# Kernel tuning notes

Hardware: AMD Instinct MI355X
Metric: run time of the kernel (lower is better)

## Reference

```python
import jax, jax.numpy as jnp
import numpy as np

# sorted irreps after merging time embedding: 144x0e + 128x1o
S = 144   # scalar (0e) multiplicity: 16 (time embedding) + 128 (node feature scalars)
V = 128   # vector (1o) multiplicity
FS = 128  # scalar part of node features
INV_SQRT3 = 1.0 / np.sqrt(3.0)  # component-normalized CG for 1o x 1o -> 0e (dot/sqrt(3))


def setup_inputs() -> dict:
    key = jax.random.key(0)
    ks = jax.random.split(key, 9)
    N = 4096
    return {
        "flat_node_features": jax.random.normal(ks[0], (N, FS + 3 * V), jnp.float32),
        "flat_times": jax.random.uniform(ks[1], (N, 1), jnp.float32),
        # time embedding o3.Linear 1x0e -> 16x0e
        "W_t": jax.random.normal(ks[2], (1, 16), jnp.float32),
        # linear_1: per-l block linear on 144x0e + 128x1o
        "W1_s": jax.random.normal(ks[3], (S, S), jnp.float32),
        "W1_v": jax.random.normal(ks[4], (V, V), jnp.float32),
        # TensorSquare path weights: strict-upper triangle = 'u<v' paths, diagonal = 'uuw' paths
        "Wss": jax.random.normal(ks[5], (S, S, S), jnp.float32),  # 0e x 0e -> 0e
        "Wsv": jax.random.normal(ks[6], (S, V, V), jnp.float32),  # 0e x 1o -> 1o ('uvw')
        "Wvv": jax.random.normal(ks[7], (V, V, S), jnp.float32),  # 1o x 1o -> 0e
        # linear_2: 128x1o -> 1x1o
        "W2": jax.random.normal(ks[8], (V, 1), jnp.float32),
    }


def _forward(feat, times, W_t, W1_s, W1_v, Wss, Wsv, Wvv, W2):
    N = feat.shape[0]
    # time embedding (fan_in = 1) + concat + (identity) permutation into sorted irreps
    emb = times @ W_t                                   # [N,16]
    s = jnp.concatenate([emb, feat[:, :FS]], axis=1)    # [N,S] scalars (0e)
    v = feat[:, FS:].reshape(N, V, 3)                   # [N,V,3] vectors (1o)

    # linear_1 (irreps-wise, fan_in normalized)
    s1 = (s @ W1_s) / np.sqrt(S)                        # [N,S]
    v1 = jnp.einsum("num,uw->nwm", v, W1_v) / np.sqrt(V)  # [N,V,3]

    # ---- TensorSquare (sorted -> sorted) ----
    mask_s = jnp.triu(jnp.ones((S, S), s1.dtype), 1)
    mask_v = jnp.triu(jnp.ones((V, V), v1.dtype), 1)

    # path A: 0e x 0e -> 0e, 'u<v'
    WssU = Wss * mask_s[:, :, None]
    tA = jnp.einsum("nvw,nv->nw", jnp.einsum("nu,uvw->nvw", s1, WssU), s1)
    tA = tA / np.sqrt(S * (S - 1) / 2)
    # path B: 0e x 0e -> 0e, 'uuw' (diagonal u==v)
    tB = jnp.einsum("nu,uw->nw", s1 * s1, jnp.einsum("uuw->uw", Wss)) / np.sqrt(S)
    # path C: 1o x 1o -> 0e, 'u<v'  (CG = dot/sqrt(3))
    D = jnp.einsum("num,nvm->nuv", v1, v1) * INV_SQRT3   # [N,V,V]
    tC = jnp.einsum("nuv,uvw->nw", D, Wvv * mask_v[:, :, None]) / np.sqrt(V * (V - 1) / 2)
    # path D: 1o x 1o -> 0e, 'uuw'
    norms = jnp.sum(v1 * v1, axis=-1) * INV_SQRT3        # [N,V]
    tD = jnp.einsum("nu,uw->nw", norms, jnp.einsum("uuw->uw", Wvv)) / np.sqrt(V)
    s2 = (tA + tB + tC + tD) / np.sqrt(4.0)              # 4 paths into 0e

    # path E: 0e x 1o -> 1o, 'uvw' (single path; CG identity under component norm)
    tmp = jnp.einsum("nu,uvw->nvw", s1, Wsv) / np.sqrt(S * V)  # [N,V,V]
    v2 = jnp.einsum("nvw,nvm->nwm", tmp, v1)             # [N,V,3]

    # gated nonlinearity: silu on scalar (l=0) channel only
    s3 = jax.nn.silu(s2)
    del s3  # scalars do not feed linear_2 (irreps_out = 1x1o has no 0e path)

    # linear_2: 128x1o -> 1x1o
    out = jnp.einsum("num,uk->nkm", v2, W2)[:, 0, :] / np.sqrt(V)  # [N,3]
    return out


def reference(flat_node_features, flat_times, W_t, W1_s, W1_v, Wss, Wsv, Wvv, W2):
    return _forward(flat_node_features, flat_times, W_t, W1_s, W1_v, Wss, Wsv, Wvv, W2)
```

## Files before the change

### kernel.cpp

```cpp
#include <hip/hip_runtime.h>
#include <hip/hip_bf16.h>
#include <math.h>


#define S 144
#define V 128

typedef __attribute__((ext_vector_type(8))) short bf16x8;
typedef __attribute__((ext_vector_type(4))) float f32x4;

__global__ __launch_bounds__(256) void k1_D(const float* __restrict__ Wsv,
                                            const float* __restrict__ W2,
                                            float* __restrict__ D) {
    const int wave = threadIdx.x >> 6;
    const int lane = threadIdx.x & 63;
    const int uv = blockIdx.x * 4 + wave;
    const float2* src = (const float2*)Wsv + (size_t)uv * 64;
    const float2* w2 = (const float2*)W2;
    float2 a = src[lane];
    float2 w = w2[lane];
    float acc = a.x * w.x + a.y * w.y;
#pragma unroll
    for (int off = 1; off < 64; off <<= 1)
        acc += __shfl_xor(acc, off, 64);
    if (lane == 0) D[uv] = acc;
}

__global__ __launch_bounds__(256) void k23_Mb(const float* __restrict__ D,
                                              const float* __restrict__ W1s,
                                              const float* __restrict__ W1v,
                                              const float* __restrict__ Wt,
                                              unsigned short* __restrict__ Mt,
                                              float* __restrict__ b) {
    __shared__ float w1v[V * 129];
    __shared__ float wrow[S];
    __shared__ float Fpart[4][V];
    __shared__ float Fsh[V];
    const int tid = threadIdx.x;
    const int q = blockIdx.x;

    {
        const float4* W1v4 = (const float4*)W1v;
        for (int i = tid; i < V * V / 4; i += 256) {
            const float4 t = W1v4[i];
            const int base = i * 4;
            float* dst = &w1v[(base >> 7) * 129 + (base & 127)];
            dst[0] = t.x; dst[1] = t.y; dst[2] = t.z; dst[3] = t.w;
        }
    }
    if (tid < S) {
        if (q < V) {
            wrow[tid] = W1s[(16 + q) * S + tid];
        } else {
            float acc = 0.f;
#pragma unroll
            for (int p = 0; p < 16; ++p)
                acc = fmaf(Wt[p], W1s[p * S + tid], acc);
            wrow[tid] = acc;
        }
    }
    __syncthreads();

    {
        const int w = tid >> 6, t = tid & 63;
        float fx = 0.f, fy = 0.f;
#pragma unroll 6
        for (int u = 36 * w; u < 36 * w + 36; ++u) {
            const float wr = wrow[u];
            const float2 dv = *(const float2*)&D[u * V + 2 * t];
            fx = fmaf(wr, dv.x, fx);
            fy = fmaf(wr, dv.y, fy);
        }
        Fpart[w][2 * t + 0] = fx;
        Fpart[w][2 * t + 1] = fy;
    }
    __syncthreads();
    if (tid < V)
        Fsh[tid] = (Fpart[0][tid] + Fpart[1][tid]) + (Fpart[2][tid] + Fpart[3][tid]);
    __syncthreads();

    if (tid < V) {
        const float scale = 1.0f / (144.0f * 128.0f * sqrtf(128.0f));
        float m0 = 0.f, m1 = 0.f, m2 = 0.f, m3 = 0.f;
#pragma unroll 8
        for (int v = 0; v < V; v += 4) {
            m0 = fmaf(Fsh[v + 0], w1v[tid * 129 + v + 0], m0);
            m1 = fmaf(Fsh[v + 1], w1v[tid * 129 + v + 1], m1);
            m2 = fmaf(Fsh[v + 2], w1v[tid * 129 + v + 2], m2);
            m3 = fmaf(Fsh[v + 3], w1v[tid * 129 + v + 3], m3);
        }
        const float r = ((m0 + m1) + (m2 + m3)) * scale;
        if (q < V) {
            const __hip_bfloat16 h = __float2bfloat16(r);
            Mt[tid * V + q] = *(const unsigned short*)&h;
        } else {
            b[tid] = r;
        }
    }
}

__global__ __launch_bounds__(256) void k4_mfma(const float* __restrict__ feat,
                                               const float* __restrict__ times,
                                               const unsigned short* __restrict__ Mtg,
                                               const float* __restrict__ bg,
                                               float* __restrict__ out) {
    __shared__ unsigned short Msh[V][136];
    __shared__ unsigned short srow[16][136];
    __shared__ float tsh[16];
    __shared__ float red[4][16][3];
    const int tid = threadIdx.x;
    const int wave = tid >> 6;
    const int lane = tid & 63;
    const int n0 = blockIdx.x * 16;

    {
        const uint4* src = (const uint4*)Mtg;
#pragma unroll
        for (int i = 0; i < 8; ++i) {
            const int idx = tid + 256 * i;
            const int r = idx >> 4;
            const int c8 = (idx & 15) * 8;
            *(uint4*)&Msh[r][c8] = src[idx];
        }
    }
    {
        const int r = tid >> 4, q0 = (tid & 15) * 8;
        const float* p = feat + (size_t)(n0 + r) * 512 + q0;
        const float4 f0 = *(const float4*)(p);
        const float4 f1 = *(const float4*)(p + 4);
        __hip_bfloat162 p0 = __float22bfloat162_rn(make_float2(f0.x, f0.y));
        __hip_bfloat162 p1 = __float22bfloat162_rn(make_float2(f0.z, f0.w));
        __hip_bfloat162 p2 = __float22bfloat162_rn(make_float2(f1.x, f1.y));
        __hip_bfloat162 p3 = __float22bfloat162_rn(make_float2(f1.z, f1.w));
        uint4 pk;
        pk.x = *(const unsigned*)&p0;
        pk.y = *(const unsigned*)&p1;
        pk.z = *(const unsigned*)&p2;
        pk.w = *(const unsigned*)&p3;
        *(uint4*)&srow[r][q0] = pk;
    }
    if (tid < 16) tsh[tid] = times[n0 + tid];
    const int mrow = lane & 15;
    const int kch = lane >> 4;
    const float bc0 = bg[32 * wave + mrow];
    const float bc1 = bg[32 * wave + 16 + mrow];
    __syncthreads();

    f32x4 acc0 = {0.f, 0.f, 0.f, 0.f};
    f32x4 acc1 = {0.f, 0.f, 0.f, 0.f};
#pragma unroll
    for (int kk = 0; kk < 4; ++kk) {
        const bf16x8 af = *(const bf16x8*)&srow[mrow][kk * 32 + kch * 8];
        const bf16x8 bf0 = *(const bf16x8*)&Msh[32 * wave + mrow][kk * 32 + kch * 8];
        const bf16x8 bf1 = *(const bf16x8*)&Msh[32 * wave + 16 + mrow][kk * 32 + kch * 8];
        acc0 = __builtin_amdgcn_mfma_f32_16x16x32_bf16(af, bf0, acc0, 0, 0, 0);
        acc1 = __builtin_amdgcn_mfma_f32_16x16x32_bf16(af, bf1, acc1, 0, 0, 0);
    }

    float pm[4][3];
#pragma unroll
    for (int i = 0; i < 4; ++i) {
        const int nr = kch * 4 + i;
        const float t = tsh[nr];
        const float h0 = acc0[i] + t * bc0;
        const float h1 = acc1[i] + t * bc1;
        const float* vp0 = feat + (size_t)(n0 + nr) * 512 + V + 3 * (32 * wave + mrow);
        const float* vp1 = vp0 + 48;
#pragma unroll
        for (int m = 0; m < 3; ++m)
            pm[i][m] = vp0[m] * h0 + vp1[m] * h1;
    }
#pragma unroll
    for (int i = 0; i < 4; ++i) {
#pragma unroll
        for (int m = 0; m < 3; ++m) {
            float v = pm[i][m];
            v += __shfl_xor(v, 1, 64);
            v += __shfl_xor(v, 2, 64);
            v += __shfl_xor(v, 4, 64);
            v += __shfl_xor(v, 8, 64);
            pm[i][m] = v;
        }
        if (mrow == 0) {
            const int nr = kch * 4 + i;
            red[wave][nr][0] = pm[i][0];
            red[wave][nr][1] = pm[i][1];
            red[wave][nr][2] = pm[i][2];
        }
    }
    __syncthreads();
    if (tid < 48) {
        const int nr = tid / 3, m = tid % 3;
        out[(size_t)(n0 + nr) * 3 + m] =
            red[0][nr][m] + red[1][nr][m] + red[2][nr][m] + red[3][nr][m];
    }
}

extern "C" void kernel_launch(void* const* d_in, const int* in_sizes, int n_in,
                              void* d_out, int out_size, void* d_ws, size_t ws_size,
                              hipStream_t stream) {
    const float* feat  = (const float*)d_in[0];
    const float* times = (const float*)d_in[1];
    const float* Wt    = (const float*)d_in[2];
    const float* W1s   = (const float*)d_in[3];
    const float* W1v   = (const float*)d_in[4];
    const float* Wsv   = (const float*)d_in[6];
    const float* W2    = (const float*)d_in[8];

    float* ws = (float*)d_ws;
    float* D  = ws;
    unsigned short* Mt = (unsigned short*)(ws + 18432);
    float* b  = ws + 18432 + 8192;

    k1_D<<<dim3(4608), dim3(256), 0, stream>>>(Wsv, W2, D);
    k23_Mb<<<dim3(129), dim3(256), 0, stream>>>(D, W1s, W1v, Wt, Mt, b);
    k4_mfma<<<dim3(256), dim3(256), 0, stream>>>(feat, times, Mt, b, (float*)d_out);
}
```

Measured before the change: 18.71 us.

## Fuse weight-reduction and M-building kernels with atomic counter handoff

Merges the Wsv·W2 reduction kernel and the M/b construction kernel into one launch. 144 producer blocks each reduce one u-slice with float4 loads, then increment a global counter. 129 consumer blocks stage W1v and wrow while producers run, and spin on the counter before reading D. This removes a kernel launch boundary and overlaps consumer staging with producer work. In exchange it adds a memset launch and relies on all producer blocks being resident or scheduled ahead of consumers to avoid deadlock.

```diff
diff --git a/kernel.cpp b/kernel.cpp
--- a/kernel.cpp
+++ b/kernel.cpp
@@ -9,92 +9,114 @@
 typedef __attribute__((ext_vector_type(8))) short bf16x8;
 typedef __attribute__((ext_vector_type(4))) float f32x4;
 
-__global__ __launch_bounds__(256) void k1_D(const float* __restrict__ Wsv,
-                                            const float* __restrict__ W2,
-                                            float* __restrict__ D) {
-    const int wave = threadIdx.x >> 6;
-    const int lane = threadIdx.x & 63;
-    const int uv = blockIdx.x * 4 + wave;
-    const float2* src = (const float2*)Wsv + (size_t)uv * 64;
-    const float2* w2 = (const float2*)W2;
-    float2 a = src[lane];
-    float2 w = w2[lane];
-    float acc = a.x * w.x + a.y * w.y;
-#pragma unroll
-    for (int off = 1; off < 64; off <<= 1)
-        acc += __shfl_xor(acc, off, 64);
-    if (lane == 0) D[uv] = acc;
-}
-
-__global__ __launch_bounds__(256) void k23_Mb(const float* __restrict__ D,
-                                              const float* __restrict__ W1s,
-                                              const float* __restrict__ W1v,
-                                              const float* __restrict__ Wt,
-                                              unsigned short* __restrict__ Mt,
-                                              float* __restrict__ b) {
+__global__ __launch_bounds__(256) void k1_DM(const float* __restrict__ Wsv,
+                                             const float* __restrict__ W2,
+                                             const float* __restrict__ W1s,
+                                             const float* __restrict__ W1v,
+                                             const float* __restrict__ Wt,
+                                             float* __restrict__ D,
+                                             unsigned short* __restrict__ Mt,
+                                             float* __restrict__ b,
+                                             unsigned* __restrict__ cnt) {
     __shared__ float w1v[V * 129];
     __shared__ float wrow[S];
     __shared__ float Fpart[4][V];
     __shared__ float Fsh[V];
     const int tid = threadIdx.x;
-    const int q = blockIdx.x;
-
-    {
-        const float4* W1v4 = (const float4*)W1v;
-        for (int i = tid; i < V * V / 4; i += 256) {
-            const float4 t = W1v4[i];
-            const int base = i * 4;
-            float* dst = &w1v[(base >> 7) * 129 + (base & 127)];
-            dst[0] = t.x; dst[1] = t.y; dst[2] = t.z; dst[3] = t.w;
-        }
-    }
-    if (tid < S) {
-        if (q < V) {
-            wrow[tid] = W1s[(16 + q) * S + tid];
-        } else {
-            float acc = 0.f;
-#pragma unroll
-            for (int p = 0; p < 16; ++p)
-                acc = fmaf(Wt[p], W1s[p * S + tid], acc);
-            wrow[tid] = acc;
-        }
-    }
-    __syncthreads();
-
-    {
-        const int w = tid >> 6, t = tid & 63;
-        float fx = 0.f, fy = 0.f;
+    const int wave = tid >> 6;
+    const int lane = tid & 63;
+
+    if (blockIdx.x < S) {
+        const int half = lane >> 5;
+        const int j = lane & 31;
+        const int u = blockIdx.x;
+        const float4* Wsv4 = (const float4*)Wsv;
+        const float4 w4 = ((const float4*)W2)[j];
+        const size_t base4 = ((size_t)u * V + 32 * wave) * 32;
+        float4 a[16];
+#pragma unroll
+        for (int i = 0; i < 16; ++i)
+            a[i] = Wsv4[base4 + (size_t)(2 * i + half) * 32 + j];
+#pragma unroll
+        for (int i = 0; i < 16; ++i) {
+            float acc = a[i].x * w4.x + a[i].y * w4.y + a[i].z * w4.z + a[i].w * w4.w;
+#pragma unroll
+            for (int off = 1; off < 32; off <<= 1)
+                acc += __shfl_xor(acc, off, 64);
+            if (j == 0) D[u * V + 32 * wave + 2 * i + half] = acc;
+        }
+        __syncthreads();
+        if (tid == 0) {
+            __threadfence();
+            __hip_atomic_fetch_add(cnt, 1u, __ATOMIC_ACQ_REL, __HIP_MEMORY_SCOPE_AGENT);
+        }
+    } else {
+        const int q = blockIdx.x - S;
+
+        {
+            const float4* W1v4 = (const float4*)W1v;
+            for (int i = tid; i < V * V / 4; i += 256) {
+                const float4 t = W1v4[i];
+                const int base = i * 4;
+                float* dst = &w1v[(base >> 7) * 129 + (base & 127)];
+                dst[0] = t.x; dst[1] = t.y; dst[2] = t.z; dst[3] = t.w;
+            }
+        }
+        if (tid < S) {
+            if (q < V) {
+                wrow[tid] = W1s[(16 + q) * S + tid];
+            } else {
+                float acc = 0.f;
+#pragma unroll
+                for (int p = 0; p < 16; ++p)
+                    acc = fmaf(Wt[p], W1s[p * S + tid], acc);
+                wrow[tid] = acc;
+            }
+        }
+        __syncthreads();
+
+        if (tid == 0) {
+            while (__hip_atomic_load(cnt, __ATOMIC_ACQUIRE, __HIP_MEMORY_SCOPE_AGENT) < (unsigned)S)
+                __builtin_amdgcn_s_sleep(2);
+            __threadfence();
+        }
+        __syncthreads();
+
+        {
+            const int w = tid >> 6, t = tid & 63;
+            float fx = 0.f, fy = 0.f;
 #pragma unroll 6
-        for (int u = 36 * w; u < 36 * w + 36; ++u) {
-            const float wr = wrow[u];
-            const float2 dv = *(const float2*)&D[u * V + 2 * t];
-            fx = fmaf(wr, dv.x, fx);
-            fy = fmaf(wr, dv.y, fy);
-        }
-        Fpart[w][2 * t + 0] = fx;
-        Fpart[w][2 * t + 1] = fy;
-    }
-    __syncthreads();
-    if (tid < V)
-        Fsh[tid] = (Fpart[0][tid] + Fpart[1][tid]) + (Fpart[2][tid] + Fpart[3][tid]);
-    __syncthreads();
-
-    if (tid < V) {
-        const float scale = 1.0f / (144.0f * 128.0f * sqrtf(128.0f));
-        float m0 = 0.f, m1 = 0.f, m2 = 0.f, m3 = 0.f;
+            for (int u = 36 * w; u < 36 * w + 36; ++u) {
+                const float wr = wrow[u];
+                const float2 dv = *(const float2*)&D[u * V + 2 * t];
+                fx = fmaf(wr, dv.x, fx);
+                fy = fmaf(wr, dv.y, fy);
+            }
+            Fpart[w][2 * t + 0] = fx;
+            Fpart[w][2 * t + 1] = fy;
+        }
+        __syncthreads();
+        if (tid < V)
+            Fsh[tid] = (Fpart[0][tid] + Fpart[1][tid]) + (Fpart[2][tid] + Fpart[3][tid]);
+        __syncthreads();
+
+        if (tid < V) {
+            const float scale = 1.0f / (144.0f * 128.0f * sqrtf(128.0f));
+            float m0 = 0.f, m1 = 0.f, m2 = 0.f, m3 = 0.f;
 #pragma unroll 8
-        for (int v = 0; v < V; v += 4) {
-            m0 = fmaf(Fsh[v + 0], w1v[tid * 129 + v + 0], m0);
-            m1 = fmaf(Fsh[v + 1], w1v[tid * 129 + v + 1], m1);
-            m2 = fmaf(Fsh[v + 2], w1v[tid * 129 + v + 2], m2);
-            m3 = fmaf(Fsh[v + 3], w1v[tid * 129 + v + 3], m3);
-        }
-        const float r = ((m0 + m1) + (m2 + m3)) * scale;
-        if (q < V) {
-            const __hip_bfloat16 h = __float2bfloat16(r);
-            Mt[tid * V + q] = *(const unsigned short*)&h;
-        } else {
-            b[tid] = r;
+            for (int v = 0; v < V; v += 4) {
+                m0 = fmaf(Fsh[v + 0], w1v[tid * 129 + v + 0], m0);
+                m1 = fmaf(Fsh[v + 1], w1v[tid * 129 + v + 1], m1);
+                m2 = fmaf(Fsh[v + 2], w1v[tid * 129 + v + 2], m2);
+                m3 = fmaf(Fsh[v + 3], w1v[tid * 129 + v + 3], m3);
+            }
+            const float r = ((m0 + m1) + (m2 + m3)) * scale;
+            if (q < V) {
+                const __hip_bfloat16 h = __float2bfloat16(r);
+                Mt[tid * V + q] = *(const unsigned short*)&h;
+            } else {
+                b[tid] = r;
+            }
         }
     }
 }
@@ -211,8 +233,10 @@
     float* D  = ws;
     unsigned short* Mt = (unsigned short*)(ws + 18432);
     float* b  = ws + 18432 + 8192;
-
-    k1_D<<<dim3(4608), dim3(256), 0, stream>>>(Wsv, W2, D);
-    k23_Mb<<<dim3(129), dim3(256), 0, stream>>>(D, W1s, W1v, Wt, Mt, b);
+    unsigned* cnt = (unsigned*)(ws + 18432 + 8192 + 128);
+
+    hipMemsetAsync(cnt, 0, sizeof(unsigned), stream);
+
+    k1_DM<<<dim3(273), dim3(256), 0, stream>>>(Wsv, W2, W1s, W1v, Wt, D, Mt, b, cnt);
     k4_mfma<<<dim3(256), dim3(256), 0, stream>>>(feat, times, Mt, b, (float*)d_out);
 }
```

After: 37.95 us. 103% more time.
